# Performance work log

Measured on AMD Instinct MI355X. Metric: run time of the kernel, lower is better.

## Reference

```python
import jax, jax.numpy as jnp
import numpy as np

B, T, D = 4, 1024, 256
H, DK, C = 8, 32, 16  # n_heads, d_key, pos-encoder hidden units
DV = D // H
NEG = -1e15
EPS_SM = 1e-5
EPS_LN = 1e-5
SLOPE = 0.01  # LeakyReLU default


def setup_inputs() -> dict:
    key = jax.random.key(0)
    ks = jax.random.split(key, 16)
    s = 0.05
    x = jax.random.normal(ks[0], (B, T, D), jnp.float32)
    src_mask = jax.random.randint(ks[1], (B, T, T), 0, 2).astype(bool)
    rel_dists = jax.random.uniform(ks[2], (B, 1, T, T), jnp.float32)
    Wq = jax.random.normal(ks[3], (H, DK, D), jnp.float32) * s
    Wk = jax.random.normal(ks[4], (H, DK, D), jnp.float32) * s
    Wv = jax.random.normal(ks[5], (H, DV, D), jnp.float32) * s
    pw1 = jax.random.normal(ks[6], (H, C), jnp.float32) * s
    pb1 = jax.random.normal(ks[7], (H, C), jnp.float32) * s
    pw2 = jax.random.normal(ks[8], (H, C), jnp.float32) * s
    pb2 = jax.random.normal(ks[9], (H,), jnp.float32) * s
    Wo = jax.random.normal(ks[10], (D, D), jnp.float32) * s
    bo = jax.random.normal(ks[11], (D,), jnp.float32) * s
    Wf = jax.random.normal(ks[12], (D, D), jnp.float32) * s
    bf = jax.random.normal(ks[13], (D,), jnp.float32) * s
    g1 = jnp.ones((D,), jnp.float32)
    beta1 = jnp.zeros((D,), jnp.float32)
    g2 = jnp.ones((D,), jnp.float32)
    beta2 = jnp.zeros((D,), jnp.float32)
    return dict(x=x, src_mask=src_mask, rel_dists=rel_dists, Wq=Wq, Wk=Wk, Wv=Wv,
                pw1=pw1, pb1=pb1, pw2=pw2, pb2=pb2, Wo=Wo, bo=bo, Wf=Wf, bf=bf,
                g1=g1, beta1=beta1, g2=g2, beta2=beta2)


def _l2norm(v):
    # F.normalize(p=2, dim=-1): v / max(||v||, 1e-12)
    n = jnp.sqrt(jnp.sum(v * v, axis=-1, keepdims=True))
    return v / jnp.maximum(n, 1e-12)


def _lrelu(h):
    return jnp.where(h >= 0, h, SLOPE * h)


def _pos_bias(d, pw1, pb1, pw2, pb2):
    # d: [B,T,T]; per-head 1x1-conv MLP applied elementwise.
    # Loop over the tiny channel dim (16) to avoid a [B,H,T,T,C] intermediate.
    bias = jnp.broadcast_to(pb2[None, :, None, None], (d.shape[0], pw1.shape[0], d.shape[1], d.shape[2]))
    for c in range(pw1.shape[1]):
        h = d[:, None] * pw1[None, :, c, None, None] + pb1[None, :, c, None, None]
        bias = bias + pw2[None, :, c, None, None] * _lrelu(h)
    return bias  # [B,H,T,T]


def _layer_norm(v, g, b):
    mu = jnp.mean(v, axis=-1, keepdims=True)
    var = jnp.mean((v - mu) ** 2, axis=-1, keepdims=True)
    return (v - mu) * jax.lax.rsqrt(var + EPS_LN) * g + b


def reference(x, src_mask, rel_dists, Wq, Wk, Wv, pw1, pb1, pw2, pb2,
              Wo, bo, Wf, bf, g1, beta1, g2, beta2):
    # cosine-normalized multi-head attention (all heads batched)
    q = _l2norm(jnp.einsum('btd,hkd->bhtk', x, Wq))
    k = _l2norm(jnp.einsum('bsd,hkd->bhsk', x, Wk))
    v = jnp.einsum('bsd,hvd->bhsv', x, Wv)
    logits = jnp.einsum('bhtk,bhsk->bhts', q, k)
    logits = logits - _pos_bias(rel_dists[:, 0], pw1, pb1, pw2, pb2)
    logits = jnp.where(src_mask[:, None], NEG, logits)
    # custom softmax: exp / (sum + 1e-5) (handles all-padded rows)
    z = jnp.exp(logits)
    attn = z / (jnp.sum(z, axis=-1, keepdims=True) + EPS_SM)
    heads = jnp.einsum('bhts,bhsv->bhtv', attn, v)
    y = heads.transpose(0, 2, 1, 3).reshape(x.shape[0], x.shape[1], -1)  # concat heads
    y = y @ Wo.T + bo
    # residual + LN + FFN (dropout is identity in eval mode)
    zz = _layer_norm(x + y, g1, beta1)
    z_ff = _lrelu(zz @ Wf.T + bf)
    return _layer_norm(zz + z_ff, g2, beta2)
```

## Files before the change

kernel.cpp:

```cpp
#include <hip/hip_runtime.h>
#include <math.h>

#define Tc 1024
#define Dc 256
#define Hc 8
#define Cc 16
#define LUTN 256

typedef __attribute__((ext_vector_type(8))) short short8;
typedef __attribute__((ext_vector_type(4))) float f32x4;

__device__ __forceinline__ unsigned bf16u(float x) {
    unsigned u = __float_as_uint(x);
    return (u + 0x7FFFu + ((u >> 16) & 1u)) >> 16;
}
__device__ __forceinline__ unsigned pk2(float lo, float hi) {
    return bf16u(lo) | (bf16u(hi) << 16);
}
__device__ __forceinline__ unsigned pk2t(float lo, float hi) {
    return __builtin_amdgcn_perm(__float_as_uint(hi), __float_as_uint(lo), 0x07060302u);
}
__device__ __forceinline__ float upk(unsigned v) { return __uint_as_float(v << 16); }
__device__ __forceinline__ float upkh(unsigned v) { return __uint_as_float(v & 0xffff0000u); }

__global__ __launch_bounds__(256) void cast_all(
    const float* __restrict__ rel, const int* __restrict__ msk,
    const float* __restrict__ Wq, const float* __restrict__ Wk,
    const float* __restrict__ Wv, const float* __restrict__ Wo,
    const float* __restrict__ Wf,
    const float* __restrict__ pw1, const float* __restrict__ pb1,
    const float* __restrict__ pw2, const float* __restrict__ pb2,
    ushort* __restrict__ Wqkvc, ushort* __restrict__ Woc,
    ushort* __restrict__ Wfc, ushort* __restrict__ LUTb,
    ushort* __restrict__ Dm)
{
    const int bid = blockIdx.x;
    const int tid = threadIdx.x;
    if (bid == 320) {
        const int bin = tid;
        const float d0 = bin * (1.f / LUTN), d1 = (bin + 1) * (1.f / LUTN);
        for (int h = 0; h < Hc; ++h) {
            float y0 = pb2[h], y1 = pb2[h];
#pragma unroll
            for (int c = 0; c < Cc; ++c) {
                float w1 = pw1[h * Cc + c], b1 = pb1[h * Cc + c], w2 = pw2[h * Cc + c];
                float h0 = fmaf(w1, d0, b1), h1 = fmaf(w1, d1, b1);
                y0 = fmaf(w2, h0 >= 0.f ? h0 : 0.01f * h0, y0);
                y1 = fmaf(w2, h1 >= 0.f ? h1 : 0.01f * h1, y1);
            }
            float a = (y1 - y0) * (float)LUTN;
            float b = y0 - a * d0;
            LUTb[(h >> 1) * 1024 + bin * 4 + (h & 1) * 2]     = (ushort)bf16u(a);
            LUTb[(h >> 1) * 1024 + bin * 4 + (h & 1) * 2 + 1] = (ushort)bf16u(b);
        }
        return;
    }
    if (bid < 320) {
        const int e = bid * 1024 + tid * 4;
        const float* src; ushort* dst; int off;
        if      (e <  65536) { src = Wq; dst = Wqkvc;          off = e; }
        else if (e < 131072) { src = Wk; dst = Wqkvc + 65536;  off = e - 65536; }
        else if (e < 196608) { src = Wv; dst = Wqkvc + 131072; off = e - 131072; }
        else if (e < 262144) { src = Wo; dst = Woc;            off = e - 196608; }
        else                 { src = Wf; dst = Wfc;            off = e - 262144; }
        float4 v = *(const float4*)(src + off);
        uint2 p; p.x = pk2(v.x, v.y); p.y = pk2(v.z, v.w);
        *(uint2*)(dst + off) = p;
        return;
    }
    const int idx = (bid - 321) * 1024 + tid * 4;
    float4 d4 = *(const float4*)(rel + idx);
    int4   m4 = *(const int4*)(msk + idx);
    uint2 p;
    p.x = (m4.x ? 0xBF80u : bf16u(d4.x)) | ((m4.y ? 0xBF80u : bf16u(d4.y)) << 16);
    p.y = (m4.z ? 0xBF80u : bf16u(d4.z)) | ((m4.w ? 0xBF80u : bf16u(d4.w)) << 16);
    *(uint2*)(Dm + idx) = p;
}

__global__ __launch_bounds__(256) void qkv_direct(
    const float* __restrict__ x, const ushort* __restrict__ Wqkv,
    ushort* __restrict__ Qb, ushort* __restrict__ Kb, ushort* __restrict__ Vt)
{
    const int tid = threadIdx.x;
    const int w = tid >> 6;
    const int l = tid & 63;
    const int u = l & 15, g = l >> 4;
    const int rbase = blockIdx.x * 16;
    const int cb = (blockIdx.y * 4 + w) * 64;

    f32x4 acc[4];
#pragma unroll
    for (int nt = 0; nt < 4; ++nt) acc[nt] = (f32x4){0.f, 0.f, 0.f, 0.f};

    const float* arow = x + (size_t)(rbase + u) * 256 + g * 8;
#pragma unroll 2
    for (int k0 = 0; k0 < 256; k0 += 32) {
        float4 a0 = *(const float4*)(arow + k0);
        float4 a1 = *(const float4*)(arow + k0 + 4);
        union { short8 s; unsigned wds[4]; } A;
        A.wds[0] = pk2(a0.x, a0.y); A.wds[1] = pk2(a0.z, a0.w);
        A.wds[2] = pk2(a1.x, a1.y); A.wds[3] = pk2(a1.z, a1.w);
#pragma unroll
        for (int nt = 0; nt < 4; ++nt) {
            short8 bfr = *(const short8*)(Wqkv + (size_t)(cb + nt * 16 + u) * 256 + k0 + g * 8);
            acc[nt] = __builtin_amdgcn_mfma_f32_16x16x32_bf16(A.s, bfr, acc[nt], 0, 0, 0);
        }
    }

    const int mat = cb >> 8;
    const int fcb = cb & 255;
    if (mat < 2) {
        ushort* Out = (mat == 0) ? Qb : Kb;
#pragma unroll
        for (int hp = 0; hp < 2; ++hp) {
            const int head = (fcb >> 5) + hp;
#pragma unroll
            for (int reg = 0; reg < 4; ++reg) {
                float ss = acc[2 * hp][reg] * acc[2 * hp][reg]
                         + acc[2 * hp + 1][reg] * acc[2 * hp + 1][reg];
                ss += __shfl_xor(ss, 1, 64);
                ss += __shfl_xor(ss, 2, 64);
                ss += __shfl_xor(ss, 4, 64);
                ss += __shfl_xor(ss, 8, 64);
                float scn = 1.f / fmaxf(sqrtf(ss), 1e-12f);
                const int t = rbase + 4 * g + reg;
                const int bb = t >> 10, tt = t & 1023;
                const size_t base = ((size_t)(bb * 8 + head) * Tc + tt) * 32;
                Out[base + u]      = (ushort)bf16u(acc[2 * hp][reg] * scn);
                Out[base + 16 + u] = (ushort)bf16u(acc[2 * hp + 1][reg] * scn);
            }
        }
    } else {
#pragma unroll
        for (int nt = 0; nt < 4; ++nt) {
            const int head = (fcb >> 5) + (nt >> 1);
            const int vt = nt & 1;
#pragma unroll
            for (int reg = 0; reg < 4; ++reg) {
                const int s = rbase + 4 * g + reg;
                const int bb = s >> 10, ss = s & 1023;
                const int bh = bb * 8 + head;
                Vt[(((size_t)bh * 32 + (ss >> 5)) * 2 + vt) * 512 + u * 32 + (ss & 31)] =
                    (ushort)bf16u(acc[nt][reg]);
            }
        }
    }
}

__global__ __launch_bounds__(256) void attn_mfma(
    const ushort* __restrict__ Qb, const ushort* __restrict__ Kb,
    const ushort* __restrict__ Vt, const ushort* __restrict__ Dm,
    const ushort* __restrict__ LUTb,
    ushort* __restrict__ Yb)
{
    const int tid = threadIdx.x;
    const int w = tid >> 6;
    const int l = tid & 63;
    const int u = l & 15;
    const int g = l >> 4;
    const int t0 = blockIdx.x * 16;
    const int b = blockIdx.y;
    const int hg = blockIdx.z;

    __shared__ __align__(16) ushort lut_s[1024];
    __shared__ __align__(16) ushort comb[4 * 16 * 72];
    __shared__ float rs_s[8 * 16];

    if (tid < 128)
        *(uint4*)(lut_s + tid * 8) = *(const uint4*)(LUTb + hg * 1024 + tid * 8);

    const int bh0 = b * 8 + hg * 2;
    short8 qf[2];
#pragma unroll
    for (int hi = 0; hi < 2; ++hi)
        qf[hi] = *(const short8*)(Qb + (((size_t)(bh0 + hi) * Tc + t0 + u) * 32 + g * 8));

    const short8 ones = (short8){0x3F80, 0x3F80, 0x3F80, 0x3F80,
                                 0x3F80, 0x3F80, 0x3F80, 0x3F80};

    f32x4 oacc[2][2];
    f32x4 rsacc[2];
#pragma unroll
    for (int hi = 0; hi < 2; ++hi) {
        oacc[hi][0] = (f32x4){0.f, 0.f, 0.f, 0.f};
        oacc[hi][1] = (f32x4){0.f, 0.f, 0.f, 0.f};
        rsacc[hi]   = (f32x4){0.f, 0.f, 0.f, 0.f};
    }

    __syncthreads();

    const int s_begin = w * 256;
    const ushort* drow = Dm + (size_t)b * Tc * Tc + (size_t)(t0 + u) * Tc;

    uint4 dmv = *(const uint4*)(drow + s_begin + 8 * g);
    short8 kc[2][2];
#pragma unroll
    for (int hi = 0; hi < 2; ++hi) {
        const size_t kb = ((size_t)(bh0 + hi) * Tc + s_begin + 2 * u) * 32 + g * 8;
        kc[hi][0] = *(const short8*)(Kb + kb);
        kc[hi][1] = *(const short8*)(Kb + kb + 32);
    }

    for (int sc = s_begin; sc < s_begin + 256; sc += 32) {
        const int nx = (sc + 32 < s_begin + 256) ? sc + 32 : s_begin;
        uint4 dmn = *(const uint4*)(drow + nx + 8 * g);
        short8 kn[2][2];
#pragma unroll
        for (int hi = 0; hi < 2; ++hi) {
            const size_t kb = ((size_t)(bh0 + hi) * Tc + nx + 2 * u) * 32 + g * 8;
            kn[hi][0] = *(const short8*)(Kb + kb);
            kn[hi][1] = *(const short8*)(Kb + kb + 32);
        }

        const unsigned dw[4] = {dmv.x, dmv.y, dmv.z, dmv.w};
        float dA[4], dB[4];
#pragma unroll
        for (int j = 0; j < 4; ++j) {
            dA[j] = upk(dw[j]);
            dB[j] = upkh(dw[j]);
        }
        float biasA[4][2], biasB[4][2];
#pragma unroll
        for (int j = 0; j < 4; ++j) {
            int iA = (int)(dA[j] * (float)LUTN);
            int iB = (int)(dB[j] * (float)LUTN);
            iA = iA < 0 ? 0 : (iA > LUTN - 1 ? LUTN - 1 : iA);
            iB = iB < 0 ? 0 : (iB > LUTN - 1 ? LUTN - 1 : iB);
            uint2 wA = *(const uint2*)(lut_s + iA * 4);
            uint2 wB = *(const uint2*)(lut_s + iB * 4);
            biasA[j][0] = fmaf(upk(wA.x), dA[j], upkh(wA.x));
            biasA[j][1] = fmaf(upk(wA.y), dA[j], upkh(wA.y));
            biasB[j][0] = fmaf(upk(wB.x), dB[j], upkh(wB.x));
            biasB[j][1] = fmaf(upk(wB.y), dB[j], upkh(wB.y));
        }
#pragma unroll
        for (int hi = 0; hi < 2; ++hi) {
            const f32x4 z4 = (f32x4){0.f, 0.f, 0.f, 0.f};
            f32x4 sA = __builtin_amdgcn_mfma_f32_16x16x32_bf16(kc[hi][0], qf[hi], z4, 0, 0, 0);
            f32x4 sB = __builtin_amdgcn_mfma_f32_16x16x32_bf16(kc[hi][1], qf[hi], z4, 0, 0, 0);
            union { short8 s; unsigned w4[4]; } P;
#pragma unroll
            for (int j = 0; j < 4; ++j) {
                float zA = (dA[j] < 0.f) ? 0.f : __expf(sA[j] - biasA[j][hi]);
                float zB = (dB[j] < 0.f) ? 0.f : __expf(sB[j] - biasB[j][hi]);
                P.w4[j] = pk2t(zA, zB);
            }
            const ushort* vb = Vt + ((size_t)(bh0 + hi) * 32 + (sc >> 5)) * 1024;
            short8 vf0 = *(const short8*)(vb + u * 32 + g * 8);
            short8 vf1 = *(const short8*)(vb + 512 + u * 32 + g * 8);
            oacc[hi][0] = __builtin_amdgcn_mfma_f32_16x16x32_bf16(P.s, vf0, oacc[hi][0], 0, 0, 0);
            oacc[hi][1] = __builtin_amdgcn_mfma_f32_16x16x32_bf16(P.s, vf1, oacc[hi][1], 0, 0, 0);
            rsacc[hi]   = __builtin_amdgcn_mfma_f32_16x16x32_bf16(P.s, ones, rsacc[hi], 0, 0, 0);
        }
        dmv = dmn;
#pragma unroll
        for (int hi = 0; hi < 2; ++hi) {
            kc[hi][0] = kn[hi][0];
            kc[hi][1] = kn[hi][1];
        }
    }

#pragma unroll
    for (int hi = 0; hi < 2; ++hi)
        if (u == 0) {
#pragma unroll
            for (int reg = 0; reg < 4; ++reg)
                rs_s[(w * 2 + hi) * 16 + 4 * g + reg] = rsacc[hi][reg];
        }
#pragma unroll
    for (int hi = 0; hi < 2; ++hi)
#pragma unroll
        for (int vt = 0; vt < 2; ++vt)
#pragma unroll
            for (int reg = 0; reg < 4; ++reg)
                comb[w * 1152 + (4 * g + reg) * 72 + hi * 32 + vt * 16 + u] =
                    (ushort)(__float_as_uint(oacc[hi][vt][reg]) >> 16);
    __syncthreads();

    if (tid < 128) {
        const int tl = tid >> 3;
        const int f0 = (tid & 7) * 8;
        const int hl = f0 >> 5;
        float rstot = rs_s[hl * 16 + tl] + rs_s[(2 + hl) * 16 + tl]
                    + rs_s[(4 + hl) * 16 + tl] + rs_s[(6 + hl) * 16 + tl];
        float inv = 1.f / (rstot + 1e-5f);
        float o[8];
#pragma unroll
        for (int k = 0; k < 8; ++k) o[k] = 0.f;
#pragma unroll
        for (int ww = 0; ww < 4; ++ww) {
            uint4 pv = *(const uint4*)&comb[ww * 1152 + tl * 72 + f0];
            o[0] += upk(pv.x); o[1] += upkh(pv.x);
            o[2] += upk(pv.y); o[3] += upkh(pv.y);
            o[4] += upk(pv.z); o[5] += upkh(pv.z);
            o[6] += upk(pv.w); o[7] += upkh(pv.w);
        }
        uint4 pwv;
        pwv.x = pk2(o[0] * inv, o[1] * inv); pwv.y = pk2(o[2] * inv, o[3] * inv);
        pwv.z = pk2(o[4] * inv, o[5] * inv); pwv.w = pk2(o[6] * inv, o[7] * inv);
        *(uint4*)(Yb + ((size_t)b * Tc + t0 + tl) * Dc + hg * 64 + f0) = pwv;
    }
}

__global__ __launch_bounds__(512) void out_fused(
    const ushort* __restrict__ Yb, const ushort* __restrict__ Woc,
    const float* __restrict__ bo, const float* __restrict__ x,
    const float* __restrict__ g1, const float* __restrict__ be1,
    const ushort* __restrict__ Wfc, const float* __restrict__ bfb,
    const float* __restrict__ g2, const float* __restrict__ be2,
    float* __restrict__ out)
{
    const int tid = threadIdx.x;
    const int w = tid >> 6;
    const int l = tid & 63;
    const int u = l & 15, g = l >> 4;
    const int rbase = blockIdx.x * 16;

    __shared__ float red1[128], red2[128];
    __shared__ __align__(16) ushort ZZs[16 * 256];

    f32x4 acc[2];
    acc[0] = (f32x4){0.f, 0.f, 0.f, 0.f};
    acc[1] = (f32x4){0.f, 0.f, 0.f, 0.f};
    const ushort* arow = Yb + (size_t)(rbase + u) * 256 + g * 8;
#pragma unroll 2
    for (int k0 = 0; k0 < 256; k0 += 32) {
        short8 af = *(const short8*)(arow + k0);
#pragma unroll
        for (int nt = 0; nt < 2; ++nt) {
            short8 bfr = *(const short8*)(Woc + (size_t)(w * 32 + nt * 16 + u) * 256 + k0 + g * 8);
            acc[nt] = __builtin_amdgcn_mfma_f32_16x16x32_bf16(af, bfr, acc[nt], 0, 0, 0);
        }
    }

    float bv[2];
#pragma unroll
    for (int nt = 0; nt < 2; ++nt) bv[nt] = bo[w * 32 + nt * 16 + u];

    float sv[4][2];
#pragma unroll
    for (int reg = 0; reg < 4; ++reg) {
        const int row = rbase + 4 * g + reg;
        float s1 = 0.f, s2 = 0.f;
#pragma unroll
        for (int nt = 0; nt < 2; ++nt) {
            const int col = w * 32 + nt * 16 + u;
            float s = acc[nt][reg] + bv[nt] + x[(size_t)row * 256 + col];
            sv[reg][nt] = s;
            s1 += s;
            s2 = fmaf(s, s, s2);
        }
        s1 += __shfl_xor(s1, 1, 64); s2 += __shfl_xor(s2, 1, 64);
        s1 += __shfl_xor(s1, 2, 64); s2 += __shfl_xor(s2, 2, 64);
        s1 += __shfl_xor(s1, 4, 64); s2 += __shfl_xor(s2, 4, 64);
        s1 += __shfl_xor(s1, 8, 64); s2 += __shfl_xor(s2, 8, 64);
        if (u == 0) { red1[w * 16 + 4 * g + reg] = s1; red2[w * 16 + 4 * g + reg] = s2; }
    }
    __syncthreads();

    float zzv[4][2];
#pragma unroll
    for (int reg = 0; reg < 4; ++reg) {
        const int rl = 4 * g + reg;
        float S1 = 0.f, S2 = 0.f;
#pragma unroll
        for (int ww = 0; ww < 8; ++ww) { S1 += red1[ww * 16 + rl]; S2 += red2[ww * 16 + rl]; }
        float mu = S1 * (1.f / 256.f);
        float var = S2 * (1.f / 256.f) - mu * mu;
        float rsig = rsqrtf(var + 1e-5f);
#pragma unroll
        for (int nt = 0; nt < 2; ++nt) {
            const int col = w * 32 + nt * 16 + u;
            float zz = (sv[reg][nt] - mu) * rsig * g1[col] + be1[col];
            zzv[reg][nt] = zz;
            const int boff = (rl * 512 + col * 2) ^ ((rl & 7) << 4);
            *(ushort*)((char*)ZZs + boff) = (ushort)bf16u(zz);
        }
    }
    __syncthreads();

    f32x4 acc2[2];
    acc2[0] = (f32x4){0.f, 0.f, 0.f, 0.f};
    acc2[1] = (f32x4){0.f, 0.f, 0.f, 0.f};
#pragma unroll 2
    for (int k0 = 0; k0 < 256; k0 += 32) {
        const int aoff = (u * 512 + (k0 + g * 8) * 2) ^ ((u & 7) << 4);
        short8 af = *(const short8*)((const char*)ZZs + aoff);
#pragma unroll
        for (int nt = 0; nt < 2; ++nt) {
            short8 bfr = *(const short8*)(Wfc + (size_t)(w * 32 + nt * 16 + u) * 256 + k0 + g * 8);
            acc2[nt] = __builtin_amdgcn_mfma_f32_16x16x32_bf16(af, bfr, acc2[nt], 0, 0, 0);
        }
    }

    float bv2[2];
#pragma unroll
    for (int nt = 0; nt < 2; ++nt) bv2[nt] = bfb[w * 32 + nt * 16 + u];

    float sv2[4][2];
#pragma unroll
    for (int reg = 0; reg < 4; ++reg) {
        float s1 = 0.f, s2 = 0.f;
#pragma unroll
        for (int nt = 0; nt < 2; ++nt) {
            float v = acc2[nt][reg] + bv2[nt];
            v = v >= 0.f ? v : 0.01f * v;
            float s = v + zzv[reg][nt];
            sv2[reg][nt] = s;
            s1 += s;
            s2 = fmaf(s, s, s2);
        }
        s1 += __shfl_xor(s1, 1, 64); s2 += __shfl_xor(s2, 1, 64);
        s1 += __shfl_xor(s1, 2, 64); s2 += __shfl_xor(s2, 2, 64);
        s1 += __shfl_xor(s1, 4, 64); s2 += __shfl_xor(s2, 4, 64);
        s1 += __shfl_xor(s1, 8, 64); s2 += __shfl_xor(s2, 8, 64);
        if (u == 0) { red1[w * 16 + 4 * g + reg] = s1; red2[w * 16 + 4 * g + reg] = s2; }
    }
    __syncthreads();

#pragma unroll
    for (int reg = 0; reg < 4; ++reg) {
        const int row = rbase + 4 * g + reg;
        const int rl = 4 * g + reg;
        float S1 = 0.f, S2 = 0.f;
#pragma unroll
        for (int ww = 0; ww < 8; ++ww) { S1 += red1[ww * 16 + rl]; S2 += red2[ww * 16 + rl]; }
        float mu = S1 * (1.f / 256.f);
        float var = S2 * (1.f / 256.f) - mu * mu;
        float rsig = rsqrtf(var + 1e-5f);
#pragma unroll
        for (int nt = 0; nt < 2; ++nt) {
            const int col = w * 32 + nt * 16 + u;
            out[(size_t)row * 256 + col] = (sv2[reg][nt] - mu) * rsig * g2[col] + be2[col];
        }
    }
}

extern "C" void kernel_launch(void* const* d_in, const int* in_sizes, int n_in,
                              void* d_out, int out_size, void* d_ws, size_t ws_size,
                              hipStream_t stream) {
    const float* x    = (const float*)d_in[0];
    const int*   mask = (const int*)d_in[1];
    const float* rel  = (const float*)d_in[2];
    const float* Wq   = (const float*)d_in[3];
    const float* Wk   = (const float*)d_in[4];
    const float* Wv   = (const float*)d_in[5];
    const float* pw1  = (const float*)d_in[6];
    const float* pb1  = (const float*)d_in[7];
    const float* pw2  = (const float*)d_in[8];
    const float* pb2  = (const float*)d_in[9];
    const float* Wo   = (const float*)d_in[10];
    const float* bo   = (const float*)d_in[11];
    const float* Wf   = (const float*)d_in[12];
    const float* bf   = (const float*)d_in[13];
    const float* g1   = (const float*)d_in[14];
    const float* be1  = (const float*)d_in[15];
    const float* g2   = (const float*)d_in[16];
    const float* be2  = (const float*)d_in[17];
    float* out = (float*)d_out;

    char* wsb = (char*)d_ws;
    ushort* Qb    = (ushort*)(wsb);
    ushort* Kb    = (ushort*)(wsb + (size_t)( 2 << 20));
    ushort* Vt    = (ushort*)(wsb + (size_t)( 4 << 20));
    ushort* Yb    = (ushort*)(wsb + (size_t)( 6 << 20));
    ushort* Wqkvc = (ushort*)(wsb + (size_t)( 8 << 20));
    ushort* Woc   = (ushort*)(wsb + (size_t)( 8 << 20) + (512 << 10));
    ushort* Wfc   = (ushort*)(wsb + (size_t)( 8 << 20) + (768 << 10));
    ushort* LUTb  = (ushort*)(wsb + (size_t)( 9 << 20));
    ushort* Dm    = (ushort*)(wsb + (size_t)(10 << 20));

    cast_all<<<4417, 256, 0, stream>>>(rel, mask, Wq, Wk, Wv, Wo, Wf,
                                       pw1, pb1, pw2, pb2,
                                       Wqkvc, Woc, Wfc, LUTb, Dm);
    qkv_direct<<<dim3(256, 3), 256, 0, stream>>>(x, Wqkvc, Qb, Kb, Vt);
    attn_mfma<<<dim3(64, 4, 4), 256, 0, stream>>>(Qb, Kb, Vt, Dm, LUTb, Yb);
    out_fused<<<256, 512, 0, stream>>>(Yb, Woc, bo, x, g1, be1,
                                       Wfc, bf, g2, be2, out);
}
```

Measured before the change: 178.8 us.

## Remove cast prepass; fuse weight casts, LUT build and mask merge into consumers

Drops the separate cast_all kernel. Weights are now converted from fp32 to bf16 on the fly inside the GEMM loops, each attention block builds its positional-bias LUT in shared memory, and the attention kernel reads the fp32 rel_dists and int mask directly instead of a pre-merged bf16 buffer. This removes one launch and the write-then-reread of a 4x1024x1024 bf16 intermediate. In exchange the attention kernel loads four times more bytes per distance/mask element, and weights are re-converted in every block.

```diff
diff --git a/kernel.cpp b/kernel.cpp
--- a/kernel.cpp
+++ b/kernel.cpp
@@ -23,62 +23,19 @@
 __device__ __forceinline__ float upk(unsigned v) { return __uint_as_float(v << 16); }
 __device__ __forceinline__ float upkh(unsigned v) { return __uint_as_float(v & 0xffff0000u); }
 
-__global__ __launch_bounds__(256) void cast_all(
-    const float* __restrict__ rel, const int* __restrict__ msk,
+__device__ __forceinline__ short8 packW8(const float* __restrict__ p) {
+    float4 b0 = *(const float4*)(p);
+    float4 b1 = *(const float4*)(p + 4);
+    union { short8 s; unsigned wds[4]; } B;
+    B.wds[0] = pk2(b0.x, b0.y); B.wds[1] = pk2(b0.z, b0.w);
+    B.wds[2] = pk2(b1.x, b1.y); B.wds[3] = pk2(b1.z, b1.w);
+    return B.s;
+}
+
+__global__ __launch_bounds__(256) void qkv_direct(
+    const float* __restrict__ x,
     const float* __restrict__ Wq, const float* __restrict__ Wk,
-    const float* __restrict__ Wv, const float* __restrict__ Wo,
-    const float* __restrict__ Wf,
-    const float* __restrict__ pw1, const float* __restrict__ pb1,
-    const float* __restrict__ pw2, const float* __restrict__ pb2,
-    ushort* __restrict__ Wqkvc, ushort* __restrict__ Woc,
-    ushort* __restrict__ Wfc, ushort* __restrict__ LUTb,
-    ushort* __restrict__ Dm)
-{
-    const int bid = blockIdx.x;
-    const int tid = threadIdx.x;
-    if (bid == 320) {
-        const int bin = tid;
-        const float d0 = bin * (1.f / LUTN), d1 = (bin + 1) * (1.f / LUTN);
-        for (int h = 0; h < Hc; ++h) {
-            float y0 = pb2[h], y1 = pb2[h];
-#pragma unroll
-            for (int c = 0; c < Cc; ++c) {
-                float w1 = pw1[h * Cc + c], b1 = pb1[h * Cc + c], w2 = pw2[h * Cc + c];
-                float h0 = fmaf(w1, d0, b1), h1 = fmaf(w1, d1, b1);
-                y0 = fmaf(w2, h0 >= 0.f ? h0 : 0.01f * h0, y0);
-                y1 = fmaf(w2, h1 >= 0.f ? h1 : 0.01f * h1, y1);
-            }
-            float a = (y1 - y0) * (float)LUTN;
-            float b = y0 - a * d0;
-            LUTb[(h >> 1) * 1024 + bin * 4 + (h & 1) * 2]     = (ushort)bf16u(a);
-            LUTb[(h >> 1) * 1024 + bin * 4 + (h & 1) * 2 + 1] = (ushort)bf16u(b);
-        }
-        return;
-    }
-    if (bid < 320) {
-        const int e = bid * 1024 + tid * 4;
-        const float* src; ushort* dst; int off;
-        if      (e <  65536) { src = Wq; dst = Wqkvc;          off = e; }
-        else if (e < 131072) { src = Wk; dst = Wqkvc + 65536;  off = e - 65536; }
-        else if (e < 196608) { src = Wv; dst = Wqkvc + 131072; off = e - 131072; }
-        else if (e < 262144) { src = Wo; dst = Woc;            off = e - 196608; }
-        else                 { src = Wf; dst = Wfc;            off = e - 262144; }
-        float4 v = *(const float4*)(src + off);
-        uint2 p; p.x = pk2(v.x, v.y); p.y = pk2(v.z, v.w);
-        *(uint2*)(dst + off) = p;
-        return;
-    }
-    const int idx = (bid - 321) * 1024 + tid * 4;
-    float4 d4 = *(const float4*)(rel + idx);
-    int4   m4 = *(const int4*)(msk + idx);
-    uint2 p;
-    p.x = (m4.x ? 0xBF80u : bf16u(d4.x)) | ((m4.y ? 0xBF80u : bf16u(d4.y)) << 16);
-    p.y = (m4.z ? 0xBF80u : bf16u(d4.z)) | ((m4.w ? 0xBF80u : bf16u(d4.w)) << 16);
-    *(uint2*)(Dm + idx) = p;
-}
-
-__global__ __launch_bounds__(256) void qkv_direct(
-    const float* __restrict__ x, const ushort* __restrict__ Wqkv,
+    const float* __restrict__ Wv,
     ushort* __restrict__ Qb, ushort* __restrict__ Kb, ushort* __restrict__ Vt)
 {
     const int tid = threadIdx.x;
@@ -87,6 +44,9 @@
     const int u = l & 15, g = l >> 4;
     const int rbase = blockIdx.x * 16;
     const int cb = (blockIdx.y * 4 + w) * 64;
+    const int mat = cb >> 8;
+    const int fcb = cb & 255;
+    const float* Wmat = (mat == 0) ? Wq : (mat == 1) ? Wk : Wv;
 
     f32x4 acc[4];
 #pragma unroll
@@ -95,20 +55,14 @@
     const float* arow = x + (size_t)(rbase + u) * 256 + g * 8;
 #pragma unroll 2
     for (int k0 = 0; k0 < 256; k0 += 32) {
-        float4 a0 = *(const float4*)(arow + k0);
-        float4 a1 = *(const float4*)(arow + k0 + 4);
-        union { short8 s; unsigned wds[4]; } A;
-        A.wds[0] = pk2(a0.x, a0.y); A.wds[1] = pk2(a0.z, a0.w);
-        A.wds[2] = pk2(a1.x, a1.y); A.wds[3] = pk2(a1.z, a1.w);
+        short8 af = packW8(arow + k0);
 #pragma unroll
         for (int nt = 0; nt < 4; ++nt) {
-            short8 bfr = *(const short8*)(Wqkv + (size_t)(cb + nt * 16 + u) * 256 + k0 + g * 8);
-            acc[nt] = __builtin_amdgcn_mfma_f32_16x16x32_bf16(A.s, bfr, acc[nt], 0, 0, 0);
-        }
-    }
-
-    const int mat = cb >> 8;
-    const int fcb = cb & 255;
+            short8 bfr = packW8(Wmat + (size_t)(fcb + nt * 16 + u) * 256 + k0 + g * 8);
+            acc[nt] = __builtin_amdgcn_mfma_f32_16x16x32_bf16(af, bfr, acc[nt], 0, 0, 0);
+        }
+    }
+
     if (mat < 2) {
         ushort* Out = (mat == 0) ? Qb : Kb;
 #pragma unroll
@@ -149,8 +103,10 @@
 
 __global__ __launch_bounds__(256) void attn_mfma(
     const ushort* __restrict__ Qb, const ushort* __restrict__ Kb,
-    const ushort* __restrict__ Vt, const ushort* __restrict__ Dm,
-    const ushort* __restrict__ LUTb,
+    const ushort* __restrict__ Vt,
+    const float* __restrict__ rel, const int* __restrict__ msk,
+    const float* __restrict__ pw1, const float* __restrict__ pb1,
+    const float* __restrict__ pw2, const float* __restrict__ pb2,
     ushort* __restrict__ Yb)
 {
     const int tid = threadIdx.x;
@@ -166,8 +122,26 @@
     __shared__ __align__(16) ushort comb[4 * 16 * 72];
     __shared__ float rs_s[8 * 16];
 
-    if (tid < 128)
-        *(uint4*)(lut_s + tid * 8) = *(const uint4*)(LUTb + hg * 1024 + tid * 8);
+    {
+        const int bin = tid;
+        const float d0 = bin * (1.f / LUTN), d1 = (bin + 1) * (1.f / LUTN);
+#pragma unroll
+        for (int hp = 0; hp < 2; ++hp) {
+            const int h = hg * 2 + hp;
+            float y0 = pb2[h], y1 = pb2[h];
+#pragma unroll
+            for (int c = 0; c < Cc; ++c) {
+                float w1 = pw1[h * Cc + c], b1 = pb1[h * Cc + c], w2 = pw2[h * Cc + c];
+                float h0 = fmaf(w1, d0, b1), h1 = fmaf(w1, d1, b1);
+                y0 = fmaf(w2, h0 >= 0.f ? h0 : 0.01f * h0, y0);
+                y1 = fmaf(w2, h1 >= 0.f ? h1 : 0.01f * h1, y1);
+            }
+            float a = (y1 - y0) * (float)LUTN;
+            float bq = y0 - a * d0;
+            lut_s[bin * 4 + hp * 2]     = (ushort)bf16u(a);
+            lut_s[bin * 4 + hp * 2 + 1] = (ushort)bf16u(bq);
+        }
+    }
 
     const int bh0 = b * 8 + hg * 2;
     short8 qf[2];
@@ -190,9 +164,13 @@
     __syncthreads();
 
     const int s_begin = w * 256;
-    const ushort* drow = Dm + (size_t)b * Tc * Tc + (size_t)(t0 + u) * Tc;
-
-    uint4 dmv = *(const uint4*)(drow + s_begin + 8 * g);
+    const float* rrow = rel + (size_t)b * Tc * Tc + (size_t)(t0 + u) * Tc;
+    const int*   mrow = msk + (size_t)b * Tc * Tc + (size_t)(t0 + u) * Tc;
+
+    float4 r0c = *(const float4*)(rrow + s_begin + 8 * g);
+    float4 r1c = *(const float4*)(rrow + s_begin + 8 * g + 4);
+    int4   m0c = *(const int4*)(mrow + s_begin + 8 * g);
+    int4   m1c = *(const int4*)(mrow + s_begin + 8 * g + 4);
     short8 kc[2][2];
 #pragma unroll
     for (int hi = 0; hi < 2; ++hi) {
@@ -203,7 +181,10 @@
 
     for (int sc = s_begin; sc < s_begin + 256; sc += 32) {
         const int nx = (sc + 32 < s_begin + 256) ? sc + 32 : s_begin;
-        uint4 dmn = *(const uint4*)(drow + nx + 8 * g);
+        float4 r0n = *(const float4*)(rrow + nx + 8 * g);
+        float4 r1n = *(const float4*)(rrow + nx + 8 * g + 4);
+        int4   m0n = *(const int4*)(mrow + nx + 8 * g);
+        int4   m1n = *(const int4*)(mrow + nx + 8 * g + 4);
         short8 kn[2][2];
 #pragma unroll
         for (int hi = 0; hi < 2; ++hi) {
@@ -212,12 +193,13 @@
             kn[hi][1] = *(const short8*)(Kb + kb + 32);
         }
 
-        const unsigned dw[4] = {dmv.x, dmv.y, dmv.z, dmv.w};
+        const float rv[8] = {r0c.x, r0c.y, r0c.z, r0c.w, r1c.x, r1c.y, r1c.z, r1c.w};
+        const int   mv[8] = {m0c.x, m0c.y, m0c.z, m0c.w, m1c.x, m1c.y, m1c.z, m1c.w};
         float dA[4], dB[4];
 #pragma unroll
         for (int j = 0; j < 4; ++j) {
-            dA[j] = upk(dw[j]);
-            dB[j] = upkh(dw[j]);
+            dA[j] = mv[2 * j]     ? -1.f : rv[2 * j];
+            dB[j] = mv[2 * j + 1] ? -1.f : rv[2 * j + 1];
         }
         float biasA[4][2], biasB[4][2];
 #pragma unroll
@@ -252,7 +234,7 @@
             oacc[hi][1] = __builtin_amdgcn_mfma_f32_16x16x32_bf16(P.s, vf1, oacc[hi][1], 0, 0, 0);
             rsacc[hi]   = __builtin_amdgcn_mfma_f32_16x16x32_bf16(P.s, ones, rsacc[hi], 0, 0, 0);
         }
-        dmv = dmn;
+        r0c = r0n; r1c = r1n; m0c = m0n; m1c = m1n;
 #pragma unroll
         for (int hi = 0; hi < 2; ++hi) {
             kc[hi][0] = kn[hi][0];
@@ -303,10 +285,10 @@
 }
 
 __global__ __launch_bounds__(512) void out_fused(
-    const ushort* __restrict__ Yb, const ushort* __restrict__ Woc,
+    const ushort* __restrict__ Yb, const float* __restrict__ Wo,
     const float* __restrict__ bo, const float* __restrict__ x,
     const float* __restrict__ g1, const float* __restrict__ be1,
-    const ushort* __restrict__ Wfc, const float* __restrict__ bfb,
+    const float* __restrict__ Wf, const float* __restrict__ bfb,
     const float* __restrict__ g2, const float* __restrict__ be2,
     float* __restrict__ out)
 {
@@ -328,7 +310,7 @@
         short8 af = *(const short8*)(arow + k0);
 #pragma unroll
         for (int nt = 0; nt < 2; ++nt) {
-            short8 bfr = *(const short8*)(Woc + (size_t)(w * 32 + nt * 16 + u) * 256 + k0 + g * 8);
+            short8 bfr = packW8(Wo + (size_t)(w * 32 + nt * 16 + u) * 256 + k0 + g * 8);
             acc[nt] = __builtin_amdgcn_mfma_f32_16x16x32_bf16(af, bfr, acc[nt], 0, 0, 0);
         }
     }
@@ -388,7 +370,7 @@
         short8 af = *(const short8*)((const char*)ZZs + aoff);
 #pragma unroll
         for (int nt = 0; nt < 2; ++nt) {
-            short8 bfr = *(const short8*)(Wfc + (size_t)(w * 32 + nt * 16 + u) * 256 + k0 + g * 8);
+            short8 bfr = packW8(Wf + (size_t)(w * 32 + nt * 16 + u) * 256 + k0 + g * 8);
             acc2[nt] = __builtin_amdgcn_mfma_f32_16x16x32_bf16(af, bfr, acc2[nt], 0, 0, 0);
         }
     }
@@ -460,21 +442,14 @@
     float* out = (float*)d_out;
 
     char* wsb = (char*)d_ws;
-    ushort* Qb    = (ushort*)(wsb);
-    ushort* Kb    = (ushort*)(wsb + (size_t)( 2 << 20));
-    ushort* Vt    = (ushort*)(wsb + (size_t)( 4 << 20));
-    ushort* Yb    = (ushort*)(wsb + (size_t)( 6 << 20));
-    ushort* Wqkvc = (ushort*)(wsb + (size_t)( 8 << 20));
-    ushort* Woc   = (ushort*)(wsb + (size_t)( 8 << 20) + (512 << 10));
-    ushort* Wfc   = (ushort*)(wsb + (size_t)( 8 << 20) + (768 << 10));
-    ushort* LUTb  = (ushort*)(wsb + (size_t)( 9 << 20));
-    ushort* Dm    = (ushort*)(wsb + (size_t)(10 << 20));
-
-    cast_all<<<4417, 256, 0, stream>>>(rel, mask, Wq, Wk, Wv, Wo, Wf,
-                                       pw1, pb1, pw2, pb2,
-                                       Wqkvc, Woc, Wfc, LUTb, Dm);
-    qkv_direct<<<dim3(256, 3), 256, 0, stream>>>(x, Wqkvc, Qb, Kb, Vt);
-    attn_mfma<<<dim3(64, 4, 4), 256, 0, stream>>>(Qb, Kb, Vt, Dm, LUTb, Yb);
-    out_fused<<<256, 512, 0, stream>>>(Yb, Woc, bo, x, g1, be1,
-                                       Wfc, bf, g2, be2, out);
-}
+    ushort* Qb = (ushort*)(wsb);
+    ushort* Kb = (ushort*)(wsb + (size_t)(2 << 20));
+    ushort* Vt = (ushort*)(wsb + (size_t)(4 << 20));
+    ushort* Yb = (ushort*)(wsb + (size_t)(6 << 20));
+
+    qkv_direct<<<dim3(256, 3), 256, 0, stream>>>(x, Wq, Wk, Wv, Qb, Kb, Vt);
+    attn_mfma<<<dim3(64, 4, 4), 256, 0, stream>>>(Qb, Kb, Vt, rel, mask,
+                                                  pw1, pb1, pw2, pb2, Yb);
+    out_fused<<<256, 512, 0, stream>>>(Yb, Wo, bo, x, g1, be1,
+                                       Wf, bf, g2, be2, out);
+}
```

New measurement: 201.2 us. 12.6% more time.

## Fuse rel-dist/mask packing and LUT build into attention kernel via LDS staging

Applied to the files above, without the earlier changes.

Removes the separate pass that packed rel_dists and the mask into a bf16 global buffer and built the position-bias LUT. The attention kernel now has 512 threads per block covering all 8 heads for a 16-row tile. Each block loads its fp32 distance and int mask rows straight into swizzled shared memory and builds the full LUT in shared memory. This drops a global write and re-read of the packed buffer (about 8 MB out and back) and stops 4 head-group blocks re-reading the same rows. In exchange each block recomputes the LUT and the kernel uses roughly 55 KB of shared memory, which may lower occupancy.

```diff
diff --git a/kernel.cpp b/kernel.cpp
--- a/kernel.cpp
+++ b/kernel.cpp
@@ -23,58 +23,32 @@
 __device__ __forceinline__ float upk(unsigned v) { return __uint_as_float(v << 16); }
 __device__ __forceinline__ float upkh(unsigned v) { return __uint_as_float(v & 0xffff0000u); }
 
-__global__ __launch_bounds__(256) void cast_all(
-    const float* __restrict__ rel, const int* __restrict__ msk,
+__device__ __forceinline__ short8 packW8(const float* __restrict__ p) {
+    float4 b0 = *(const float4*)(p);
+    float4 b1 = *(const float4*)(p + 4);
+    union { short8 s; unsigned wds[4]; } B;
+    B.wds[0] = pk2(b0.x, b0.y); B.wds[1] = pk2(b0.z, b0.w);
+    B.wds[2] = pk2(b1.x, b1.y); B.wds[3] = pk2(b1.z, b1.w);
+    return B.s;
+}
+
+__global__ __launch_bounds__(256) void cast_w(
     const float* __restrict__ Wq, const float* __restrict__ Wk,
     const float* __restrict__ Wv, const float* __restrict__ Wo,
     const float* __restrict__ Wf,
-    const float* __restrict__ pw1, const float* __restrict__ pb1,
-    const float* __restrict__ pw2, const float* __restrict__ pb2,
     ushort* __restrict__ Wqkvc, ushort* __restrict__ Woc,
-    ushort* __restrict__ Wfc, ushort* __restrict__ LUTb,
-    ushort* __restrict__ Dm)
+    ushort* __restrict__ Wfc)
 {
-    const int bid = blockIdx.x;
-    const int tid = threadIdx.x;
-    if (bid == 320) {
-        const int bin = tid;
-        const float d0 = bin * (1.f / LUTN), d1 = (bin + 1) * (1.f / LUTN);
-        for (int h = 0; h < Hc; ++h) {
-            float y0 = pb2[h], y1 = pb2[h];
-#pragma unroll
-            for (int c = 0; c < Cc; ++c) {
-                float w1 = pw1[h * Cc + c], b1 = pb1[h * Cc + c], w2 = pw2[h * Cc + c];
-                float h0 = fmaf(w1, d0, b1), h1 = fmaf(w1, d1, b1);
-                y0 = fmaf(w2, h0 >= 0.f ? h0 : 0.01f * h0, y0);
-                y1 = fmaf(w2, h1 >= 0.f ? h1 : 0.01f * h1, y1);
-            }
-            float a = (y1 - y0) * (float)LUTN;
-            float b = y0 - a * d0;
-            LUTb[(h >> 1) * 1024 + bin * 4 + (h & 1) * 2]     = (ushort)bf16u(a);
-            LUTb[(h >> 1) * 1024 + bin * 4 + (h & 1) * 2 + 1] = (ushort)bf16u(b);
-        }
-        return;
-    }
-    if (bid < 320) {
-        const int e = bid * 1024 + tid * 4;
-        const float* src; ushort* dst; int off;
-        if      (e <  65536) { src = Wq; dst = Wqkvc;          off = e; }
-        else if (e < 131072) { src = Wk; dst = Wqkvc + 65536;  off = e - 65536; }
-        else if (e < 196608) { src = Wv; dst = Wqkvc + 131072; off = e - 131072; }
-        else if (e < 262144) { src = Wo; dst = Woc;            off = e - 196608; }
-        else                 { src = Wf; dst = Wfc;            off = e - 262144; }
-        float4 v = *(const float4*)(src + off);
-        uint2 p; p.x = pk2(v.x, v.y); p.y = pk2(v.z, v.w);
-        *(uint2*)(dst + off) = p;
-        return;
-    }
-    const int idx = (bid - 321) * 1024 + tid * 4;
-    float4 d4 = *(const float4*)(rel + idx);
-    int4   m4 = *(const int4*)(msk + idx);
-    uint2 p;
-    p.x = (m4.x ? 0xBF80u : bf16u(d4.x)) | ((m4.y ? 0xBF80u : bf16u(d4.y)) << 16);
-    p.y = (m4.z ? 0xBF80u : bf16u(d4.z)) | ((m4.w ? 0xBF80u : bf16u(d4.w)) << 16);
-    *(uint2*)(Dm + idx) = p;
+    const int e = blockIdx.x * 1024 + threadIdx.x * 4;
+    const float* src; ushort* dst; int off;
+    if      (e <  65536) { src = Wq; dst = Wqkvc;          off = e; }
+    else if (e < 131072) { src = Wk; dst = Wqkvc + 65536;  off = e - 65536; }
+    else if (e < 196608) { src = Wv; dst = Wqkvc + 131072; off = e - 131072; }
+    else if (e < 262144) { src = Wo; dst = Woc;            off = e - 196608; }
+    else                 { src = Wf; dst = Wfc;            off = e - 262144; }
+    float4 v = *(const float4*)(src + off);
+    uint2 p; p.x = pk2(v.x, v.y); p.y = pk2(v.z, v.w);
+    *(uint2*)(dst + off) = p;
 }
 
 __global__ __launch_bounds__(256) void qkv_direct(
@@ -95,15 +69,11 @@
     const float* arow = x + (size_t)(rbase + u) * 256 + g * 8;
 #pragma unroll 2
     for (int k0 = 0; k0 < 256; k0 += 32) {
-        float4 a0 = *(const float4*)(arow + k0);
-        float4 a1 = *(const float4*)(arow + k0 + 4);
-        union { short8 s; unsigned wds[4]; } A;
-        A.wds[0] = pk2(a0.x, a0.y); A.wds[1] = pk2(a0.z, a0.w);
-        A.wds[2] = pk2(a1.x, a1.y); A.wds[3] = pk2(a1.z, a1.w);
+        short8 af = packW8(arow + k0);
 #pragma unroll
         for (int nt = 0; nt < 4; ++nt) {
             short8 bfr = *(const short8*)(Wqkv + (size_t)(cb + nt * 16 + u) * 256 + k0 + g * 8);
-            acc[nt] = __builtin_amdgcn_mfma_f32_16x16x32_bf16(A.s, bfr, acc[nt], 0, 0, 0);
+            acc[nt] = __builtin_amdgcn_mfma_f32_16x16x32_bf16(af, bfr, acc[nt], 0, 0, 0);
         }
     }
 
@@ -147,10 +117,12 @@
     }
 }
 
-__global__ __launch_bounds__(256) void attn_mfma(
+__global__ __launch_bounds__(512) void attn_fused(
     const ushort* __restrict__ Qb, const ushort* __restrict__ Kb,
-    const ushort* __restrict__ Vt, const ushort* __restrict__ Dm,
-    const ushort* __restrict__ LUTb,
+    const ushort* __restrict__ Vt,
+    const float* __restrict__ rel, const int* __restrict__ msk,
+    const float* __restrict__ pw1, const float* __restrict__ pb1,
+    const float* __restrict__ pw2, const float* __restrict__ pb2,
     ushort* __restrict__ Yb)
 {
     const int tid = threadIdx.x;
@@ -158,18 +130,62 @@
     const int l = tid & 63;
     const int u = l & 15;
     const int g = l >> 4;
-    const int t0 = blockIdx.x * 16;
-    const int b = blockIdx.y;
-    const int hg = blockIdx.z;
-
-    __shared__ __align__(16) ushort lut_s[1024];
-    __shared__ __align__(16) ushort comb[4 * 16 * 72];
-    __shared__ float rs_s[8 * 16];
-
-    if (tid < 128)
-        *(uint4*)(lut_s + tid * 8) = *(const uint4*)(LUTb + hg * 1024 + tid * 8);
-
-    const int bh0 = b * 8 + hg * 2;
+    const int bid = blockIdx.x;
+    const int b   = (bid >> 1) & 3;
+    const int tt  = (bid >> 3) * 2 + (bid & 1);
+    const int t0  = tt * 16;
+
+    __shared__ __align__(16) ushort dm_s[16 * 1024];
+    __shared__ __align__(16) ushort lut_s[256 * 16];
+    __shared__ __align__(16) ushort comb[8 * 16 * 64];
+    __shared__ float rs_s[8 * 2 * 16];
+
+    {
+        const int bin = tid & 255;
+        const int hb  = (tid >> 8) * 4;
+        const float d0 = bin * (1.f / LUTN), d1 = (bin + 1) * (1.f / LUTN);
+#pragma unroll
+        for (int hp = 0; hp < 4; ++hp) {
+            const int h = hb + hp;
+            float y0 = pb2[h], y1 = pb2[h];
+#pragma unroll
+            for (int cc = 0; cc < Cc; ++cc) {
+                float w1 = pw1[h * Cc + cc], b1 = pb1[h * Cc + cc], w2 = pw2[h * Cc + cc];
+                float h0 = fmaf(w1, d0, b1), h1 = fmaf(w1, d1, b1);
+                y0 = fmaf(w2, h0 >= 0.f ? h0 : 0.01f * h0, y0);
+                y1 = fmaf(w2, h1 >= 0.f ? h1 : 0.01f * h1, y1);
+            }
+            float a = (y1 - y0) * (float)LUTN;
+            float bq = y0 - a * d0;
+            lut_s[bin * 16 + h * 2]     = (ushort)bf16u(a);
+            lut_s[bin * 16 + h * 2 + 1] = (ushort)bf16u(bq);
+        }
+    }
+
+    {
+        const int row = tid >> 5;
+        const int lc  = tid & 31;
+        const float* rrow = rel + ((size_t)b * Tc + t0 + row) * Tc;
+        const int*   mrow = msk + ((size_t)b * Tc + t0 + row) * Tc;
+        const int swz = (row & 7) << 4;
+#pragma unroll
+        for (int i = 0; i < 4; ++i) {
+            const int s0 = lc * 8 + i * 256;
+            float4 d0v = *(const float4*)(rrow + s0);
+            float4 d1v = *(const float4*)(rrow + s0 + 4);
+            int4   m0v = *(const int4*)(mrow + s0);
+            int4   m1v = *(const int4*)(mrow + s0 + 4);
+            uint4 p;
+            p.x = (m0v.x ? 0xBF80u : bf16u(d0v.x)) | ((m0v.y ? 0xBF80u : bf16u(d0v.y)) << 16);
+            p.y = (m0v.z ? 0xBF80u : bf16u(d0v.z)) | ((m0v.w ? 0xBF80u : bf16u(d0v.w)) << 16);
+            p.z = (m1v.x ? 0xBF80u : bf16u(d1v.x)) | ((m1v.y ? 0xBF80u : bf16u(d1v.y)) << 16);
+            p.w = (m1v.z ? 0xBF80u : bf16u(d1v.z)) | ((m1v.w ? 0xBF80u : bf16u(d1v.w)) << 16);
+            *(uint4*)((char*)dm_s + ((row * 2048 + s0 * 2) ^ swz)) = p;
+        }
+    }
+
+    const int hgp = w >> 1;
+    const int bh0 = b * 8 + hgp * 2;
     short8 qf[2];
 #pragma unroll
     for (int hi = 0; hi < 2; ++hi)
@@ -189,10 +205,9 @@
 
     __syncthreads();
 
-    const int s_begin = w * 256;
-    const ushort* drow = Dm + (size_t)b * Tc * Tc + (size_t)(t0 + u) * Tc;
-
-    uint4 dmv = *(const uint4*)(drow + s_begin + 8 * g);
+    const int s_begin = (w & 1) * 512;
+    const int dswz = (u & 7) << 4;
+
     short8 kc[2][2];
 #pragma unroll
     for (int hi = 0; hi < 2; ++hi) {
@@ -201,9 +216,8 @@
         kc[hi][1] = *(const short8*)(Kb + kb + 32);
     }
 
-    for (int sc = s_begin; sc < s_begin + 256; sc += 32) {
-        const int nx = (sc + 32 < s_begin + 256) ? sc + 32 : s_begin;
-        uint4 dmn = *(const uint4*)(drow + nx + 8 * g);
+    for (int sc = s_begin; sc < s_begin + 512; sc += 32) {
+        const int nx = (sc + 32 < s_begin + 512) ? sc + 32 : s_begin;
         short8 kn[2][2];
 #pragma unroll
         for (int hi = 0; hi < 2; ++hi) {
@@ -212,6 +226,7 @@
             kn[hi][1] = *(const short8*)(Kb + kb + 32);
         }
 
+        uint4 dmv = *(const uint4*)((const char*)dm_s + ((u * 2048 + (sc + 8 * g) * 2) ^ dswz));
         const unsigned dw[4] = {dmv.x, dmv.y, dmv.z, dmv.w};
         float dA[4], dB[4];
 #pragma unroll
@@ -226,8 +241,8 @@
             int iB = (int)(dB[j] * (float)LUTN);
             iA = iA < 0 ? 0 : (iA > LUTN - 1 ? LUTN - 1 : iA);
             iB = iB < 0 ? 0 : (iB > LUTN - 1 ? LUTN - 1 : iB);
-            uint2 wA = *(const uint2*)(lut_s + iA * 4);
-            uint2 wB = *(const uint2*)(lut_s + iB * 4);
+            uint2 wA = *(const uint2*)(lut_s + iA * 16 + hgp * 4);
+            uint2 wB = *(const uint2*)(lut_s + iB * 16 + hgp * 4);
             biasA[j][0] = fmaf(upk(wA.x), dA[j], upkh(wA.x));
             biasA[j][1] = fmaf(upk(wA.y), dA[j], upkh(wA.y));
             biasB[j][0] = fmaf(upk(wB.x), dB[j], upkh(wB.x));
@@ -252,7 +267,6 @@
             oacc[hi][1] = __builtin_amdgcn_mfma_f32_16x16x32_bf16(P.s, vf1, oacc[hi][1], 0, 0, 0);
             rsacc[hi]   = __builtin_amdgcn_mfma_f32_16x16x32_bf16(P.s, ones, rsacc[hi], 0, 0, 0);
         }
-        dmv = dmn;
 #pragma unroll
         for (int hi = 0; hi < 2; ++hi) {
             kc[hi][0] = kn[hi][0];
@@ -273,32 +287,29 @@
         for (int vt = 0; vt < 2; ++vt)
 #pragma unroll
             for (int reg = 0; reg < 4; ++reg)
-                comb[w * 1152 + (4 * g + reg) * 72 + hi * 32 + vt * 16 + u] =
+                comb[w * 1024 + (4 * g + reg) * 64 + hi * 32 + vt * 16 + u] =
                     (ushort)(__float_as_uint(oacc[hi][vt][reg]) >> 16);
     __syncthreads();
 
-    if (tid < 128) {
-        const int tl = tid >> 3;
-        const int f0 = (tid & 7) * 8;
-        const int hl = f0 >> 5;
-        float rstot = rs_s[hl * 16 + tl] + rs_s[(2 + hl) * 16 + tl]
-                    + rs_s[(4 + hl) * 16 + tl] + rs_s[(6 + hl) * 16 + tl];
+    {
+        const int tl = tid >> 5;
+        const int f0 = (tid & 31) * 8;
+        const int hgp2 = f0 >> 6;
+        const int hi = (f0 >> 5) & 1;
+        const int w0 = hgp2 * 2, w1 = w0 + 1;
+        float rstot = rs_s[(w0 * 2 + hi) * 16 + tl] + rs_s[(w1 * 2 + hi) * 16 + tl];
         float inv = 1.f / (rstot + 1e-5f);
+        uint4 pv0 = *(const uint4*)&comb[w0 * 1024 + tl * 64 + (f0 & 63)];
+        uint4 pv1 = *(const uint4*)&comb[w1 * 1024 + tl * 64 + (f0 & 63)];
         float o[8];
-#pragma unroll
-        for (int k = 0; k < 8; ++k) o[k] = 0.f;
-#pragma unroll
-        for (int ww = 0; ww < 4; ++ww) {
-            uint4 pv = *(const uint4*)&comb[ww * 1152 + tl * 72 + f0];
-            o[0] += upk(pv.x); o[1] += upkh(pv.x);
-            o[2] += upk(pv.y); o[3] += upkh(pv.y);
-            o[4] += upk(pv.z); o[5] += upkh(pv.z);
-            o[6] += upk(pv.w); o[7] += upkh(pv.w);
-        }
+        o[0] = upk(pv0.x) + upk(pv1.x);  o[1] = upkh(pv0.x) + upkh(pv1.x);
+        o[2] = upk(pv0.y) + upk(pv1.y);  o[3] = upkh(pv0.y) + upkh(pv1.y);
+        o[4] = upk(pv0.z) + upk(pv1.z);  o[5] = upkh(pv0.z) + upkh(pv1.z);
+        o[6] = upk(pv0.w) + upk(pv1.w);  o[7] = upkh(pv0.w) + upkh(pv1.w);
         uint4 pwv;
         pwv.x = pk2(o[0] * inv, o[1] * inv); pwv.y = pk2(o[2] * inv, o[3] * inv);
         pwv.z = pk2(o[4] * inv, o[5] * inv); pwv.w = pk2(o[6] * inv, o[7] * inv);
-        *(uint4*)(Yb + ((size_t)b * Tc + t0 + tl) * Dc + hg * 64 + f0) = pwv;
+        *(uint4*)(Yb + ((size_t)b * Tc + t0 + tl) * Dc + f0) = pwv;
     }
 }
 
@@ -461,20 +472,17 @@
 
     char* wsb = (char*)d_ws;
     ushort* Qb    = (ushort*)(wsb);
-    ushort* Kb    = (ushort*)(wsb + (size_t)( 2 << 20));
-    ushort* Vt    = (ushort*)(wsb + (size_t)( 4 << 20));
-    ushort* Yb    = (ushort*)(wsb + (size_t)( 6 << 20));
-    ushort* Wqkvc = (ushort*)(wsb + (size_t)( 8 << 20));
-    ushort* Woc   = (ushort*)(wsb + (size_t)( 8 << 20) + (512 << 10));
-    ushort* Wfc   = (ushort*)(wsb + (size_t)( 8 << 20) + (768 << 10));
-    ushort* LUTb  = (ushort*)(wsb + (size_t)( 9 << 20));
-    ushort* Dm    = (ushort*)(wsb + (size_t)(10 << 20));
-
-    cast_all<<<4417, 256, 0, stream>>>(rel, mask, Wq, Wk, Wv, Wo, Wf,
-                                       pw1, pb1, pw2, pb2,
-                                       Wqkvc, Woc, Wfc, LUTb, Dm);
+    ushort* Kb    = (ushort*)(wsb + (size_t)(2 << 20));
+    ushort* Vt    = (ushort*)(wsb + (size_t)(4 << 20));
+    ushort* Yb    = (ushort*)(wsb + (size_t)(6 << 20));
+    ushort* Wqkvc = (ushort*)(wsb + (size_t)(8 << 20));
+    ushort* Woc   = (ushort*)(wsb + (size_t)(8 << 20) + (512 << 10));
+    ushort* Wfc   = (ushort*)(wsb + (size_t)(8 << 20) + (768 << 10));
+
+    cast_w<<<320, 256, 0, stream>>>(Wq, Wk, Wv, Wo, Wf, Wqkvc, Woc, Wfc);
     qkv_direct<<<dim3(256, 3), 256, 0, stream>>>(x, Wqkvc, Qb, Kb, Vt);
-    attn_mfma<<<dim3(64, 4, 4), 256, 0, stream>>>(Qb, Kb, Vt, Dm, LUTb, Yb);
+    attn_fused<<<256, 512, 0, stream>>>(Qb, Kb, Vt, rel, mask,
+                                        pw1, pb1, pw2, pb2, Yb);
     out_fused<<<256, 512, 0, stream>>>(Yb, Woc, bo, x, g1, be1,
                                        Wfc, bf, g2, be2, out);
 }
```

New measurement: 170.3 us. -4.7%, faster.
